# Performance work log

Hardware: AMD Instinct MI355X
Metric: run time of the kernel (lower is better)

## Reference

```python
import jax, jax.numpy as jnp
import numpy as np

B, S, H, N_NODE = 4096, 50, 128, 50000
STDV = 1.0 / np.sqrt(H)


def _uniform(key, shape):
    return jax.random.uniform(key, shape, jnp.float32, -STDV, STDV)


def setup_inputs() -> dict:
    key = jax.random.key(0)
    ks = jax.random.split(key, 14)
    inputs = jax.random.randint(ks[0], (B, S), 0, N_NODE)
    A = jax.random.uniform(ks[1], (B, S, 2 * S), jnp.float32)
    return {
        "inputs": inputs,
        "A": A,
        "emb": _uniform(ks[2], (N_NODE, H)),
        "W_in": _uniform(ks[3], (H, H)),
        "b_in": _uniform(ks[4], (H,)),
        "W_out": _uniform(ks[5], (H, H)),
        "b_out": _uniform(ks[6], (H,)),
        "w_ih": _uniform(ks[7], (3 * H, 2 * H)),
        "b_ih": _uniform(ks[8], (3 * H,)),
        "w_hh": _uniform(ks[9], (3 * H, H)),
        "b_hh": _uniform(ks[10], (3 * H,)),
        "b_iah": _uniform(ks[11], (H,)),
        "b_oah": _uniform(ks[12], (H,)),
    }


def reference(inputs, A, emb, W_in, b_in, W_out, b_out, w_ih, b_ih, w_hh, b_hh, b_iah, b_oah):
    hidden = emb[inputs]                      # [B,S,H]
    s = A.shape[1]
    A_in, A_out = A[:, :, :s], A[:, :, s:2 * s]
    # edge-wise linear projections then adjacency aggregation
    h_in = jnp.einsum('bsh,gh->bsg', hidden, W_in) + b_in
    h_out = jnp.einsum('bsh,gh->bsg', hidden, W_out) + b_out
    input_in = jnp.matmul(A_in, h_in) + b_iah    # [B,S,H]
    input_out = jnp.matmul(A_out, h_out) + b_oah # [B,S,H]
    inp = jnp.concatenate([input_in, input_out], axis=2)  # [B,S,2H]
    gi = jnp.einsum('bsi,gi->bsg', inp, w_ih) + b_ih       # [B,S,3H]
    gh = jnp.einsum('bsh,gh->bsg', hidden, w_hh) + b_hh    # [B,S,3H]
    i_r, i_i, i_n = jnp.split(gi, 3, axis=2)
    h_r, h_i, h_n = jnp.split(gh, 3, axis=2)
    resetgate = jax.nn.sigmoid(i_r + h_r)
    inputgate = jax.nn.sigmoid(i_i + h_i)
    newgate = jnp.tanh(i_n + resetgate * h_n)
    hy = newgate + inputgate * (hidden - newgate)
    return hy
```

## Files before the change

kernel.cpp:

```cpp
#include <hip/hip_runtime.h>
#include <stdint.h>

typedef unsigned short u16;
typedef unsigned int u32;
typedef unsigned long long u64;
typedef __attribute__((ext_vector_type(2))) float f32x2;
typedef __attribute__((ext_vector_type(4))) float f32x4;
typedef __attribute__((ext_vector_type(8))) short s16x8;
typedef __attribute__((ext_vector_type(4))) u16 u16x4;
typedef __attribute__((ext_vector_type(2))) u32 u32x2;
typedef __attribute__((ext_vector_type(4))) u32 u32x4;

#define NS 50
#define NH 128

#define HT_OFF 0
#define HTP 1792
#define M_OFF  14336
#define RS_OFF 39936
#define LDS_TOTAL 40448

__device__ __forceinline__ u16 f2bf(float f) {
  u32 u = __builtin_bit_cast(u32, f);
  u32 r = (u + 0x7FFFu + ((u >> 16) & 1u)) >> 16;
  return (u16)r;
}
__device__ __forceinline__ float bf2f(u16 u) {
  return __builtin_bit_cast(float, (u32)u << 16);
}
__device__ __forceinline__ float sigm(float x) { return 1.0f / (1.0f + __expf(-x)); }
__device__ __forceinline__ float tanh_(float x) { return 1.0f - 2.0f / (1.0f + __expf(2.0f * x)); }
__device__ __forceinline__ s16x8 pack8(f32x4 a, f32x4 b) {
  s16x8 r;
  r[0] = (short)f2bf(a[0]); r[1] = (short)f2bf(a[1]);
  r[2] = (short)f2bf(a[2]); r[3] = (short)f2bf(a[3]);
  r[4] = (short)f2bf(b[0]); r[5] = (short)f2bf(b[1]);
  r[6] = (short)f2bf(b[2]); r[7] = (short)f2bf(b[3]);
  return r;
}
__device__ __forceinline__ s16x8 afrag_tr2(const unsigned char* p) {
  u32x2 a, b;
  asm volatile(
      "ds_read_b64_tr_b16 %0, %2\n\t"
      "ds_read_b64_tr_b16 %1, %2 offset:128\n\t"
      "s_waitcnt lgkmcnt(0)"
      : "=&v"(a), "=&v"(b)
      : "v"((const __attribute__((address_space(3))) unsigned char*)p)
      : "memory");
  __builtin_amdgcn_sched_barrier(0);
  u32x4 t; t[0] = a[0]; t[1] = a[1]; t[2] = b[0]; t[3] = b[1];
  return __builtin_bit_cast(s16x8, t);
}
__device__ __forceinline__ s16x8 load_outfrag(const float* ap, int kbase) {
  f32x4 x = {0.f, 0.f, 0.f, 0.f}, y = {0.f, 0.f, 0.f, 0.f};
  const float* p = ap + 50 + kbase;
  if (kbase <= 40) {
    f32x2 a0 = *(const f32x2*)(p);
    f32x2 a1 = *(const f32x2*)(p + 2);
    f32x2 a2 = *(const f32x2*)(p + 4);
    f32x2 a3 = *(const f32x2*)(p + 6);
    x[0] = a0[0]; x[1] = a0[1]; x[2] = a1[0]; x[3] = a1[1];
    y[0] = a2[0]; y[1] = a2[1]; y[2] = a3[0]; y[3] = a3[1];
  } else if (kbase == 48) {
    f32x2 a0 = *(const f32x2*)(p);
    x[0] = a0[0]; x[1] = a0[1];
  }
  return pack8(x, y);
}

__device__ __forceinline__ int upack_pos(int j, int k) {
  int kt4 = k >> 5, g4 = (k >> 3) & 3, e2 = k & 7;
  int chunk;
  if (j < 768) {
    int big = j >= 384;
    int jj = j - big * 384;
    int gate = jj >> 7, jr = jj & 127;
    chunk = ((big * 3 + gate) * 8 + (jr >> 4)) * 4 + kt4;
    return chunk * 512 + ((g4 * 16 + (jr & 15)) * 8 + e2);
  } else {
    int jj = j - 768;
    int gate = jj >> 7, jr = jj & 127;
    chunk = 192 + (gate * 8 + (jr >> 4)) * 4 + kt4;
    return chunk * 512 + ((g4 * 16 + (jr & 15)) * 8 + e2);
  }
}

__global__ __launch_bounds__(256) void k1_prep(
    const float* __restrict__ W_in, const float* __restrict__ b_in,
    const float* __restrict__ W_out, const float* __restrict__ b_out,
    const float* __restrict__ w_ih, const float* __restrict__ b_ih,
    const float* __restrict__ w_hh,
    const float* __restrict__ b_iah, const float* __restrict__ b_oah,
    u16* __restrict__ Upk, float* __restrict__ cvec)
{
  int e = blockIdx.x * 256 + threadIdx.x;
  if (e < 147456) {
    int j = e >> 7, k = e & 127;
    float s = 0.f;
    if (j < 768) {
      const float* wr = w_ih + (size_t)(j < 384 ? j : j - 384) * 256 + (j < 384 ? 0 : 128);
      const float* Wc = (j < 384 ? W_in : W_out) + k;
      #pragma unroll 8
      for (int h = 0; h < 128; ++h) s += wr[h] * Wc[h * 128];
    } else {
      s = w_hh[(size_t)(j - 768) * 128 + k];
    }
    Upk[upack_pos(j, k)] = f2bf(s);
  } else if (e < 147456 + 1152) {
    int e2 = e - 147456;
    int which = e2 / 384, g = e2 - which * 384;
    const float* wr = w_ih + (size_t)g * 256;
    float s = 0.f;
    if (which == 0) { for (int h = 0; h < 128; ++h) s += wr[h] * b_in[h]; }
    else if (which == 1) { for (int h = 0; h < 128; ++h) s += wr[128 + h] * b_out[h]; }
    else {
      for (int h = 0; h < 128; ++h) s += wr[h] * b_iah[h] + wr[128 + h] * b_oah[h];
      s += b_ih[g];
    }
    cvec[which * 384 + g] = s;
  }
}

__global__ __launch_bounds__(256, 2) void k3_main(
    const int* __restrict__ inputs, const float* __restrict__ A,
    const u16* __restrict__ Upk, const float* __restrict__ cvec,
    const float* __restrict__ emb, const float* __restrict__ b_hh,
    float* __restrict__ out)
{
  __shared__ __align__(128) unsigned char Sb[LDS_TOTAL];

  const int tid = threadIdx.x;
  const int b = blockIdx.x;
  const int w = tid >> 6, l = tid & 63;
  const int l16 = l & 15, g4 = l >> 4;

  const float* Ab = A + (size_t)b * (NS * 2 * NS);
  const int* inp = inputs + b * NS;
  float* outB = out + (size_t)b * NS * NH;
  float* rs = (float*)(Sb + RS_OFF);

  if (tid < 100) {
    int s = tid < 50 ? tid : tid - 50;
    const float* ap = Ab + s * 100;
    float sum;
    if (tid < 50) {
      f32x4 a4 = *(const f32x4*)ap;
      #pragma unroll
      for (int q = 1; q < 12; ++q) a4 += *(const f32x4*)(ap + q * 4);
      f32x4 vt = *(const f32x4*)(ap + 48);
      sum = (a4[0] + a4[1]) + (a4[2] + a4[3]) + vt[0] + vt[1];
    } else {
      f32x4 vt = *(const f32x4*)(ap + 48);
      f32x4 a4 = *(const f32x4*)(ap + 52);
      #pragma unroll
      for (int q = 1; q < 12; ++q) a4 += *(const f32x4*)(ap + 52 + q * 4);
      sum = (a4[0] + a4[1]) + (a4[2] + a4[3]) + vt[2] + vt[3];
    }
    rs[(tid < 50 ? 0 : 64) + s] = sum;
  }

  if (tid < 96) {
    int hc = tid / 12, q = tid - hc * 12;
    u32x4 z = {0, 0, 0, 0};
    *(u32x4*)(Sb + HT_OFF + hc * HTP + 1600 + q * 16) = z;
  }

  #pragma unroll
  for (int i = 0; i < 7; ++i) {
    int slot = i * 256 + tid;
    if (slot < 1600) {
      int t = slot >> 5, hch = slot & 31;
      int node = inp[t];
      f32x4 v = *(const f32x4*)(emb + (size_t)node * NH + hch * 4);
      u32 lo = (u32)f2bf(v[0]) | ((u32)f2bf(v[1]) << 16);
      u32 hi = (u32)f2bf(v[2]) | ((u32)f2bf(v[3]) << 16);
      u32x2 pv = {lo, hi};
      *(u32x2*)(Sb + HT_OFF + (hch >> 2) * HTP + (t >> 2) * 128 + (t & 3) * 32 + (hch & 3) * 8) = pv;
    }
  }

  s16x8 BfIn[4][2];
  #pragma unroll
  for (int nt = 0; nt < 4; ++nt) {
    int s = nt * 16 + l16; if (s > NS - 1) s = NS - 1;
    const float* ap = Ab + s * 100;
    {
      f32x4 x = *(const f32x4*)(ap + g4 * 8);
      f32x4 y = *(const f32x4*)(ap + g4 * 8 + 4);
      BfIn[nt][0] = pack8(x, y);
    }
    {
      f32x4 x = *(const f32x4*)(ap + 32 + g4 * 8);
      f32x4 y = *(const f32x4*)(ap + 32 + g4 * 8 + 4);
      int tb = 32 + g4 * 8;
      #pragma unroll
      for (int j = 0; j < 4; ++j) {
        if (tb + j >= NS) x[j] = 0.f;
        if (tb + 4 + j >= NS) y[j] = 0.f;
      }
      BfIn[nt][1] = pack8(x, y);
    }
  }
  __syncthreads();

  const s16x8 zero8 = {0, 0, 0, 0, 0, 0, 0, 0};

  #pragma unroll
  for (int ht2 = 0; ht2 < 2; ++ht2) {
    const int htile = w * 2 + ht2;
    f32x4 accM[2][4] = {};
    #pragma unroll
    for (int kt = 0; kt < 2; ++kt) {
      const bool ztail = (kt == 1) && (g4 == 3);
      int tile = kt * 8 + 2 * g4;
      s16x8 Af = afrag_tr2(Sb + HT_OFF + htile * HTP + (ztail ? 0 : tile * 128) + l16 * 8);
      if (ztail) Af = zero8;
      #pragma unroll
      for (int nt = 0; nt < 4; ++nt)
        accM[0][nt] = __builtin_amdgcn_mfma_f32_16x16x32_bf16(Af, BfIn[nt][kt], accM[0][nt], 0, 0, 0);
      #pragma unroll
      for (int nt = 0; nt < 4; ++nt) {
        int s = nt * 16 + l16; if (s > NS - 1) s = NS - 1;
        s16x8 Bo = load_outfrag(Ab + s * 100, kt * 32 + g4 * 8);
        accM[1][nt] = __builtin_amdgcn_mfma_f32_16x16x32_bf16(Af, Bo, accM[1][nt], 0, 0, 0);
      }
    }
    #pragma unroll
    for (int mo = 0; mo < 2; ++mo)
      #pragma unroll
      for (int nt = 0; nt < 4; ++nt) {
        int s = nt * 16 + l16;
        if (s < NS) {
          u32 colb = (u32)((mo * 128 + htile * 16 + g4 * 4) * 2);
          u32 swz = (u32)((s & 7) << 4);
          u32 lo = (u32)f2bf(accM[mo][nt][0]) | ((u32)f2bf(accM[mo][nt][1]) << 16);
          u32 hi = (u32)f2bf(accM[mo][nt][2]) | ((u32)f2bf(accM[mo][nt][3]) << 16);
          u32x2 pv = {lo, hi};
          *(u32x2*)(Sb + M_OFF + s * 512 + (colb ^ swz)) = pv;
        }
      }
  }
  __syncthreads();

  const u16* upLane = Upk + (size_t)l * 8;
  #pragma unroll
  for (int ht = 0; ht < 2; ++ht) {
    const int hb = w * 32 + ht * 16;
    const int js = w * 2 + ht;
    f32x4 acc2[3][4] = {};
    f32x4 acc3[3][4] = {};
    __builtin_amdgcn_s_setprio(1);
    #pragma unroll
    for (int kt = 0; kt < 8; ++kt) {
      s16x8 Bm[4];
      #pragma unroll
      for (int nt = 0; nt < 4; ++nt) {
        int s = nt * 16 + l16; if (s > NS - 1) s = NS - 1;
        Bm[nt] = *(const s16x8*)(Sb + M_OFF + s * 512 +
                                 ((u32)(kt * 64 + g4 * 16) ^ (u32)((s & 7) << 4)));
      }
      const int big = kt >> 2, kt4 = kt & 3;
      #pragma unroll
      for (int gate = 0; gate < 3; ++gate) {
        int chunk = ((big * 3 + gate) * 8 + js) * 4 + kt4;
        s16x8 Au = *(const s16x8*)(upLane + chunk * 512);
        #pragma unroll
        for (int nt = 0; nt < 4; ++nt)
          acc2[gate][nt] = __builtin_amdgcn_mfma_f32_16x16x32_bf16(Au, Bm[nt], acc2[gate][nt], 0, 0, 0);
      }
    }
    #pragma unroll
    for (int kt = 0; kt < 4; ++kt) {
      s16x8 Bh[4];
      #pragma unroll
      for (int nt = 0; nt < 4; ++nt) {
        int s = nt * 16 + l16; if (s > NS - 1) s = NS - 1;
        int h = kt * 32 + g4 * 8;
        Bh[nt] = *(const s16x8*)(Sb + HT_OFF + (h >> 4) * HTP + (s >> 2) * 128 +
                                 (s & 3) * 32 + (h & 15) * 2);
      }
      #pragma unroll
      for (int gate = 0; gate < 3; ++gate) {
        int chunk = 192 + (gate * 8 + js) * 4 + kt;
        s16x8 Au = *(const s16x8*)(upLane + chunk * 512);
        #pragma unroll
        for (int nt = 0; nt < 4; ++nt)
          acc3[gate][nt] = __builtin_amdgcn_mfma_f32_16x16x32_bf16(Au, Bh[nt], acc3[gate][nt], 0, 0, 0);
      }
    }
    __builtin_amdgcn_s_setprio(0);

    const int h0 = hb + g4 * 4;
    f32x4 cin[3], cou[3], cz[3], bh[3];
    #pragma unroll
    for (int gate = 0; gate < 3; ++gate) {
      int g = gate * 128 + h0;
      cin[gate] = *(const f32x4*)(cvec + g);
      cou[gate] = *(const f32x4*)(cvec + 384 + g);
      cz[gate]  = *(const f32x4*)(cvec + 768 + g);
      bh[gate]  = *(const f32x4*)(b_hh + g);
    }
    #pragma unroll
    for (int nt = 0; nt < 4; ++nt) {
      int s = nt * 16 + l16;
      int sc = s > NS - 1 ? NS - 1 : s;
      u16x4 hid4 = *(const u16x4*)(Sb + HT_OFF + (h0 >> 4) * HTP + (sc >> 2) * 128 +
                                   (sc & 3) * 32 + (h0 & 15) * 2);
      float rin = rs[sc], rou = rs[64 + sc];
      f32x4 res;
      #pragma unroll
      for (int r = 0; r < 4; ++r) {
        float gr_ = acc3[0][nt][r] + bh[0][r];
        float gi_ = acc3[1][nt][r] + bh[1][r];
        float gn_ = acc3[2][nt][r] + bh[2][r];
        float vr = acc2[0][nt][r] + rin * cin[0][r] + rou * cou[0][r] + cz[0][r] + gr_;
        float vi = acc2[1][nt][r] + rin * cin[1][r] + rou * cou[1][r] + cz[1][r] + gi_;
        float vn = acc2[2][nt][r] + rin * cin[2][r] + rou * cou[2][r] + cz[2][r];
        float rr = sigm(vr);
        float ii = sigm(vi);
        float nn = tanh_(vn + rr * gn_);
        res[r] = nn + ii * (bf2f(hid4[r]) - nn);
      }
      if (s < NS)
        *(f32x4*)(outB + (size_t)s * NH + h0) = res;
    }
  }
}

extern "C" void kernel_launch(void* const* d_in, const int* in_sizes, int n_in,
                              void* d_out, int out_size, void* d_ws, size_t ws_size,
                              hipStream_t stream) {
  const int*   inputs = (const int*)  d_in[0];
  const float* A      = (const float*)d_in[1];
  const float* emb    = (const float*)d_in[2];
  const float* W_in   = (const float*)d_in[3];
  const float* b_in   = (const float*)d_in[4];
  const float* W_out  = (const float*)d_in[5];
  const float* b_out  = (const float*)d_in[6];
  const float* w_ih   = (const float*)d_in[7];
  const float* b_ih   = (const float*)d_in[8];
  const float* w_hh   = (const float*)d_in[9];
  const float* b_hh   = (const float*)d_in[10];
  const float* b_iah  = (const float*)d_in[11];
  const float* b_oah  = (const float*)d_in[12];

  u16*   Upk  = (u16*)d_ws;
  float* cvec = (float*)((char*)d_ws + 294912);

  k1_prep<<<dim3(581), dim3(256), 0, stream>>>(W_in, b_in, W_out, b_out, w_ih, b_ih,
                                               w_hh, b_iah, b_oah, Upk, cvec);
  k3_main<<<dim3(4096), dim3(256), 0, stream>>>(inputs, A, Upk, cvec, emb, b_hh,
                                                (float*)d_out);
}
```

Measured before the change: 225.8 us.

## Process two batch items per block to raise MFMA N-tile utilisation

Each block now handles two sequences (100 rows), so the second-stage GEMM uses 7 N-tiles of 16 instead of 4 per sequence. This cuts padding waste from 64-of-50 to 112-of-100, and each weight fragment loaded from global memory is reused across twice as many rows. The r and i gate accumulators for the M and hidden GEMMs are merged into one set, and A fragments are packed to bf16 by truncation with perm instead of round-to-nearest. In exchange LDS doubles to about 80KB per block and register pressure grows, which can lower occupancy below the 2-blocks-per-CU launch bound. Truncation also slightly changes numerics.

```diff
diff --git a/kernel.cpp b/kernel.cpp
--- a/kernel.cpp
+++ b/kernel.cpp
@@ -14,11 +14,11 @@
 #define NS 50
 #define NH 128
 
-#define HT_OFF 0
+#define HTB 14336
 #define HTP 1792
-#define M_OFF  14336
-#define RS_OFF 39936
-#define LDS_TOTAL 40448
+#define M_OFF  28672
+#define RS_OFF 79872
+#define LDS_TOTAL 80896
 
 __device__ __forceinline__ u16 f2bf(float f) {
   u32 u = __builtin_bit_cast(u32, f);
@@ -30,13 +30,15 @@
 }
 __device__ __forceinline__ float sigm(float x) { return 1.0f / (1.0f + __expf(-x)); }
 __device__ __forceinline__ float tanh_(float x) { return 1.0f - 2.0f / (1.0f + __expf(2.0f * x)); }
-__device__ __forceinline__ s16x8 pack8(f32x4 a, f32x4 b) {
-  s16x8 r;
-  r[0] = (short)f2bf(a[0]); r[1] = (short)f2bf(a[1]);
-  r[2] = (short)f2bf(a[2]); r[3] = (short)f2bf(a[3]);
-  r[4] = (short)f2bf(b[0]); r[5] = (short)f2bf(b[1]);
-  r[6] = (short)f2bf(b[2]); r[7] = (short)f2bf(b[3]);
-  return r;
+__device__ __forceinline__ s16x8 pack8_trunc(f32x4 a, f32x4 b) {
+  u32x4 ua = __builtin_bit_cast(u32x4, a);
+  u32x4 ub = __builtin_bit_cast(u32x4, b);
+  u32x4 t;
+  t[0] = __builtin_amdgcn_perm(ua[1], ua[0], 0x07060302u);
+  t[1] = __builtin_amdgcn_perm(ua[3], ua[2], 0x07060302u);
+  t[2] = __builtin_amdgcn_perm(ub[1], ub[0], 0x07060302u);
+  t[3] = __builtin_amdgcn_perm(ub[3], ub[2], 0x07060302u);
+  return __builtin_bit_cast(s16x8, t);
 }
 __device__ __forceinline__ s16x8 afrag_tr2(const unsigned char* p) {
   u32x2 a, b;
@@ -65,7 +67,7 @@
     f32x2 a0 = *(const f32x2*)(p);
     x[0] = a0[0]; x[1] = a0[1];
   }
-  return pack8(x, y);
+  return pack8_trunc(x, y);
 }
 
 __device__ __forceinline__ int upack_pos(int j, int k) {
@@ -130,115 +132,121 @@
   __shared__ __align__(128) unsigned char Sb[LDS_TOTAL];
 
   const int tid = threadIdx.x;
-  const int b = blockIdx.x;
+  const int b2 = blockIdx.x * 2;
   const int w = tid >> 6, l = tid & 63;
   const int l16 = l & 15, g4 = l >> 4;
 
-  const float* Ab = A + (size_t)b * (NS * 2 * NS);
-  const int* inp = inputs + b * NS;
-  float* outB = out + (size_t)b * NS * NH;
   float* rs = (float*)(Sb + RS_OFF);
 
-  if (tid < 100) {
-    int s = tid < 50 ? tid : tid - 50;
-    const float* ap = Ab + s * 100;
+  if (tid < 200) {
+    int q = tid >= 100;
+    int u = tid - 100 * q;
+    int s = u >= 50 ? u - 50 : u;
+    const float* ap = A + (size_t)(b2 + q) * 5000 + s * 100;
     float sum;
-    if (tid < 50) {
+    if (u < 50) {
       f32x4 a4 = *(const f32x4*)ap;
       #pragma unroll
-      for (int q = 1; q < 12; ++q) a4 += *(const f32x4*)(ap + q * 4);
+      for (int p = 1; p < 12; ++p) a4 += *(const f32x4*)(ap + p * 4);
       f32x4 vt = *(const f32x4*)(ap + 48);
       sum = (a4[0] + a4[1]) + (a4[2] + a4[3]) + vt[0] + vt[1];
     } else {
       f32x4 vt = *(const f32x4*)(ap + 48);
       f32x4 a4 = *(const f32x4*)(ap + 52);
       #pragma unroll
-      for (int q = 1; q < 12; ++q) a4 += *(const f32x4*)(ap + 52 + q * 4);
+      for (int p = 1; p < 12; ++p) a4 += *(const f32x4*)(ap + 52 + p * 4);
       sum = (a4[0] + a4[1]) + (a4[2] + a4[3]) + vt[2] + vt[3];
     }
-    rs[(tid < 50 ? 0 : 64) + s] = sum;
-  }
-
-  if (tid < 96) {
-    int hc = tid / 12, q = tid - hc * 12;
+    rs[q * 128 + (u >= 50) * 64 + s] = sum;
+  }
+
+  if (tid < 192) {
+    int q = tid / 96, r2 = tid - q * 96;
+    int hc = r2 / 12, off = (r2 - hc * 12) * 16;
     u32x4 z = {0, 0, 0, 0};
-    *(u32x4*)(Sb + HT_OFF + hc * HTP + 1600 + q * 16) = z;
+    *(u32x4*)(Sb + q * HTB + hc * HTP + 1600 + off) = z;
   }
 
   #pragma unroll
-  for (int i = 0; i < 7; ++i) {
+  for (int i = 0; i < 13; ++i) {
     int slot = i * 256 + tid;
-    if (slot < 1600) {
-      int t = slot >> 5, hch = slot & 31;
-      int node = inp[t];
+    if (slot < 3200) {
+      int q = slot >= 1600;
+      int rem = slot - 1600 * q;
+      int t = rem >> 5, hch = rem & 31;
+      int node = inputs[(b2 + q) * NS + t];
       f32x4 v = *(const f32x4*)(emb + (size_t)node * NH + hch * 4);
       u32 lo = (u32)f2bf(v[0]) | ((u32)f2bf(v[1]) << 16);
       u32 hi = (u32)f2bf(v[2]) | ((u32)f2bf(v[3]) << 16);
       u32x2 pv = {lo, hi};
-      *(u32x2*)(Sb + HT_OFF + (hch >> 2) * HTP + (t >> 2) * 128 + (t & 3) * 32 + (hch & 3) * 8) = pv;
-    }
-  }
-
-  s16x8 BfIn[4][2];
+      *(u32x2*)(Sb + q * HTB + (hch >> 2) * HTP + (t >> 2) * 128 + (t & 3) * 32 + (hch & 3) * 8) = pv;
+    }
+  }
+  __syncthreads();
+
+  const s16x8 zero8 = {0, 0, 0, 0, 0, 0, 0, 0};
+
   #pragma unroll
-  for (int nt = 0; nt < 4; ++nt) {
-    int s = nt * 16 + l16; if (s > NS - 1) s = NS - 1;
-    const float* ap = Ab + s * 100;
-    {
-      f32x4 x = *(const f32x4*)(ap + g4 * 8);
-      f32x4 y = *(const f32x4*)(ap + g4 * 8 + 4);
-      BfIn[nt][0] = pack8(x, y);
-    }
-    {
-      f32x4 x = *(const f32x4*)(ap + 32 + g4 * 8);
-      f32x4 y = *(const f32x4*)(ap + 32 + g4 * 8 + 4);
-      int tb = 32 + g4 * 8;
-      #pragma unroll
-      for (int j = 0; j < 4; ++j) {
-        if (tb + j >= NS) x[j] = 0.f;
-        if (tb + 4 + j >= NS) y[j] = 0.f;
-      }
-      BfIn[nt][1] = pack8(x, y);
-    }
-  }
-  __syncthreads();
-
-  const s16x8 zero8 = {0, 0, 0, 0, 0, 0, 0, 0};
-
-  #pragma unroll
-  for (int ht2 = 0; ht2 < 2; ++ht2) {
-    const int htile = w * 2 + ht2;
-    f32x4 accM[2][4] = {};
-    #pragma unroll
-    for (int kt = 0; kt < 2; ++kt) {
-      const bool ztail = (kt == 1) && (g4 == 3);
-      int tile = kt * 8 + 2 * g4;
-      s16x8 Af = afrag_tr2(Sb + HT_OFF + htile * HTP + (ztail ? 0 : tile * 128) + l16 * 8);
-      if (ztail) Af = zero8;
-      #pragma unroll
-      for (int nt = 0; nt < 4; ++nt)
-        accM[0][nt] = __builtin_amdgcn_mfma_f32_16x16x32_bf16(Af, BfIn[nt][kt], accM[0][nt], 0, 0, 0);
-      #pragma unroll
-      for (int nt = 0; nt < 4; ++nt) {
-        int s = nt * 16 + l16; if (s > NS - 1) s = NS - 1;
-        s16x8 Bo = load_outfrag(Ab + s * 100, kt * 32 + g4 * 8);
-        accM[1][nt] = __builtin_amdgcn_mfma_f32_16x16x32_bf16(Af, Bo, accM[1][nt], 0, 0, 0);
-      }
-    }
-    #pragma unroll
-    for (int mo = 0; mo < 2; ++mo)
-      #pragma unroll
-      for (int nt = 0; nt < 4; ++nt) {
-        int s = nt * 16 + l16;
-        if (s < NS) {
-          u32 colb = (u32)((mo * 128 + htile * 16 + g4 * 4) * 2);
-          u32 swz = (u32)((s & 7) << 4);
-          u32 lo = (u32)f2bf(accM[mo][nt][0]) | ((u32)f2bf(accM[mo][nt][1]) << 16);
-          u32 hi = (u32)f2bf(accM[mo][nt][2]) | ((u32)f2bf(accM[mo][nt][3]) << 16);
-          u32x2 pv = {lo, hi};
-          *(u32x2*)(Sb + M_OFF + s * 512 + (colb ^ swz)) = pv;
-        }
-      }
+  for (int q = 0; q < 2; ++q) {
+    const float* Aq = A + (size_t)(b2 + q) * 5000;
+    s16x8 BfIn[4][2];
+    #pragma unroll
+    for (int nt = 0; nt < 4; ++nt) {
+      int s = nt * 16 + l16; if (s > NS - 1) s = NS - 1;
+      const float* ap = Aq + s * 100;
+      {
+        f32x4 x = *(const f32x4*)(ap + g4 * 8);
+        f32x4 y = *(const f32x4*)(ap + g4 * 8 + 4);
+        BfIn[nt][0] = pack8_trunc(x, y);
+      }
+      {
+        f32x4 x = *(const f32x4*)(ap + 32 + g4 * 8);
+        f32x4 y = *(const f32x4*)(ap + 32 + g4 * 8 + 4);
+        int tb = 32 + g4 * 8;
+        #pragma unroll
+        for (int j = 0; j < 4; ++j) {
+          if (tb + j >= NS) x[j] = 0.f;
+          if (tb + 4 + j >= NS) y[j] = 0.f;
+        }
+        BfIn[nt][1] = pack8_trunc(x, y);
+      }
+    }
+    #pragma unroll
+    for (int ht2 = 0; ht2 < 2; ++ht2) {
+      const int htile = w * 2 + ht2;
+      f32x4 accM[2][4] = {};
+      #pragma unroll
+      for (int kt = 0; kt < 2; ++kt) {
+        const bool ztail = (kt == 1) && (g4 == 3);
+        int tile = kt * 8 + 2 * g4;
+        s16x8 Af = afrag_tr2(Sb + q * HTB + htile * HTP + (ztail ? 0 : tile * 128) + l16 * 8);
+        if (ztail) Af = zero8;
+        #pragma unroll
+        for (int nt = 0; nt < 4; ++nt)
+          accM[0][nt] = __builtin_amdgcn_mfma_f32_16x16x32_bf16(Af, BfIn[nt][kt], accM[0][nt], 0, 0, 0);
+        #pragma unroll
+        for (int nt = 0; nt < 4; ++nt) {
+          int s = nt * 16 + l16; if (s > NS - 1) s = NS - 1;
+          s16x8 Bo = load_outfrag(Aq + s * 100, kt * 32 + g4 * 8);
+          accM[1][nt] = __builtin_amdgcn_mfma_f32_16x16x32_bf16(Af, Bo, accM[1][nt], 0, 0, 0);
+        }
+      }
+      #pragma unroll
+      for (int mo = 0; mo < 2; ++mo)
+        #pragma unroll
+        for (int nt = 0; nt < 4; ++nt) {
+          int s = nt * 16 + l16;
+          if (s < NS) {
+            int r = s + 50 * q;
+            u32 colb = (u32)((mo * 128 + htile * 16 + g4 * 4) * 2);
+            u32 swz = (u32)((r & 7) << 4);
+            u32 lo = (u32)f2bf(accM[mo][nt][0]) | ((u32)f2bf(accM[mo][nt][1]) << 16);
+            u32 hi = (u32)f2bf(accM[mo][nt][2]) | ((u32)f2bf(accM[mo][nt][3]) << 16);
+            u32x2 pv = {lo, hi};
+            *(u32x2*)(Sb + M_OFF + r * 512 + (colb ^ swz)) = pv;
+          }
+        }
+    }
   }
   __syncthreads();
 
@@ -247,45 +255,59 @@
   for (int ht = 0; ht < 2; ++ht) {
     const int hb = w * 32 + ht * 16;
     const int js = w * 2 + ht;
-    f32x4 acc2[3][4] = {};
-    f32x4 acc3[3][4] = {};
+    f32x4 accRI[2][7] = {};
+    f32x4 accN2[7] = {};
+    f32x4 accN3[7] = {};
     __builtin_amdgcn_s_setprio(1);
     #pragma unroll
     for (int kt = 0; kt < 8; ++kt) {
-      s16x8 Bm[4];
-      #pragma unroll
-      for (int nt = 0; nt < 4; ++nt) {
-        int s = nt * 16 + l16; if (s > NS - 1) s = NS - 1;
-        Bm[nt] = *(const s16x8*)(Sb + M_OFF + s * 512 +
-                                 ((u32)(kt * 64 + g4 * 16) ^ (u32)((s & 7) << 4)));
+      s16x8 Bm[7];
+      #pragma unroll
+      for (int nt = 0; nt < 7; ++nt) {
+        int r = nt * 16 + l16; if (r > 99) r = 99;
+        Bm[nt] = *(const s16x8*)(Sb + M_OFF + r * 512 +
+                                 ((u32)(kt * 64 + g4 * 16) ^ (u32)((r & 7) << 4)));
       }
       const int big = kt >> 2, kt4 = kt & 3;
       #pragma unroll
       for (int gate = 0; gate < 3; ++gate) {
         int chunk = ((big * 3 + gate) * 8 + js) * 4 + kt4;
         s16x8 Au = *(const s16x8*)(upLane + chunk * 512);
-        #pragma unroll
-        for (int nt = 0; nt < 4; ++nt)
-          acc2[gate][nt] = __builtin_amdgcn_mfma_f32_16x16x32_bf16(Au, Bm[nt], acc2[gate][nt], 0, 0, 0);
+        if (gate < 2) {
+          #pragma unroll
+          for (int nt = 0; nt < 7; ++nt)
+            accRI[gate][nt] = __builtin_amdgcn_mfma_f32_16x16x32_bf16(Au, Bm[nt], accRI[gate][nt], 0, 0, 0);
+        } else {
+          #pragma unroll
+          for (int nt = 0; nt < 7; ++nt)
+            accN2[nt] = __builtin_amdgcn_mfma_f32_16x16x32_bf16(Au, Bm[nt], accN2[nt], 0, 0, 0);
+        }
       }
     }
     #pragma unroll
     for (int kt = 0; kt < 4; ++kt) {
-      s16x8 Bh[4];
-      #pragma unroll
-      for (int nt = 0; nt < 4; ++nt) {
-        int s = nt * 16 + l16; if (s > NS - 1) s = NS - 1;
+      s16x8 Bh[7];
+      #pragma unroll
+      for (int nt = 0; nt < 7; ++nt) {
+        int r = nt * 16 + l16; if (r > 99) r = 99;
+        int q = r >= 50, s = r - 50 * q;
         int h = kt * 32 + g4 * 8;
-        Bh[nt] = *(const s16x8*)(Sb + HT_OFF + (h >> 4) * HTP + (s >> 2) * 128 +
+        Bh[nt] = *(const s16x8*)(Sb + q * HTB + (h >> 4) * HTP + (s >> 2) * 128 +
                                  (s & 3) * 32 + (h & 15) * 2);
       }
       #pragma unroll
       for (int gate = 0; gate < 3; ++gate) {
         int chunk = 192 + (gate * 8 + js) * 4 + kt;
         s16x8 Au = *(const s16x8*)(upLane + chunk * 512);
-        #pragma unroll
-        for (int nt = 0; nt < 4; ++nt)
-          acc3[gate][nt] = __builtin_amdgcn_mfma_f32_16x16x32_bf16(Au, Bh[nt], acc3[gate][nt], 0, 0, 0);
+        if (gate < 2) {
+          #pragma unroll
+          for (int nt = 0; nt < 7; ++nt)
+            accRI[gate][nt] = __builtin_amdgcn_mfma_f32_16x16x32_bf16(Au, Bh[nt], accRI[gate][nt], 0, 0, 0);
+        } else {
+          #pragma unroll
+          for (int nt = 0; nt < 7; ++nt)
+            accN3[nt] = __builtin_amdgcn_mfma_f32_16x16x32_bf16(Au, Bh[nt], accN3[nt], 0, 0, 0);
+        }
       }
     }
     __builtin_amdgcn_s_setprio(0);
@@ -301,28 +323,27 @@
       bh[gate]  = *(const f32x4*)(b_hh + g);
     }
     #pragma unroll
-    for (int nt = 0; nt < 4; ++nt) {
-      int s = nt * 16 + l16;
-      int sc = s > NS - 1 ? NS - 1 : s;
-      u16x4 hid4 = *(const u16x4*)(Sb + HT_OFF + (h0 >> 4) * HTP + (sc >> 2) * 128 +
-                                   (sc & 3) * 32 + (h0 & 15) * 2);
-      float rin = rs[sc], rou = rs[64 + sc];
+    for (int nt = 0; nt < 7; ++nt) {
+      int r = nt * 16 + l16;
+      int rc = r > 99 ? 99 : r;
+      int q = rc >= 50, s = rc - 50 * q;
+      u16x4 hid4 = *(const u16x4*)(Sb + q * HTB + (h0 >> 4) * HTP + (s >> 2) * 128 +
+                                   (s & 3) * 32 + (h0 & 15) * 2);
+      float rin = rs[q * 128 + s], rou = rs[q * 128 + 64 + s];
       f32x4 res;
       #pragma unroll
-      for (int r = 0; r < 4; ++r) {
-        float gr_ = acc3[0][nt][r] + bh[0][r];
-        float gi_ = acc3[1][nt][r] + bh[1][r];
-        float gn_ = acc3[2][nt][r] + bh[2][r];
-        float vr = acc2[0][nt][r] + rin * cin[0][r] + rou * cou[0][r] + cz[0][r] + gr_;
-        float vi = acc2[1][nt][r] + rin * cin[1][r] + rou * cou[1][r] + cz[1][r] + gi_;
-        float vn = acc2[2][nt][r] + rin * cin[2][r] + rou * cou[2][r] + cz[2][r];
+      for (int e = 0; e < 4; ++e) {
+        float vr = accRI[0][nt][e] + rin * cin[0][e] + rou * cou[0][e] + cz[0][e] + bh[0][e];
+        float vi = accRI[1][nt][e] + rin * cin[1][e] + rou * cou[1][e] + cz[1][e] + bh[1][e];
+        float vn = accN2[nt][e] + rin * cin[2][e] + rou * cou[2][e] + cz[2][e];
+        float gn_ = accN3[nt][e] + bh[2][e];
         float rr = sigm(vr);
         float ii = sigm(vi);
         float nn = tanh_(vn + rr * gn_);
-        res[r] = nn + ii * (bf2f(hid4[r]) - nn);
-      }
-      if (s < NS)
-        *(f32x4*)(outB + (size_t)s * NH + h0) = res;
+        res[e] = nn + ii * (bf2f(hid4[e]) - nn);
+      }
+      if (r < 100)
+        *(f32x4*)(out + ((size_t)(b2 + q) * NS + s) * NH + h0) = res;
     }
   }
 }
@@ -349,6 +370,6 @@
 
   k1_prep<<<dim3(581), dim3(256), 0, stream>>>(W_in, b_in, W_out, b_out, w_ih, b_ih,
                                                w_hh, b_iah, b_oah, Upk, cvec);
-  k3_main<<<dim3(4096), dim3(256), 0, stream>>>(inputs, A, Upk, cvec, emb, b_hh,
+  k3_main<<<dim3(2048), dim3(256), 0, stream>>>(inputs, A, Upk, cvec, emb, b_hh,
                                                 (float*)d_out);
 }
```

New measurement: 228.5 us. About the same (+1.2%).
